# Optimization experiments

Hardware: AMD Instinct MI355X
Metric: run time of the kernel (lower is better)

The kernel has to match this reference:

```python
import jax, jax.numpy as jnp
import numpy as np

B, N, T, E, EH, C = 32, 500, 13, 2000, 300, 40
EPS = 1e-5


def _bn_noaffine(x):
    m = x.mean(axis=(0, 2, 3), keepdims=True)
    v = x.var(axis=(0, 2, 3), keepdims=True)
    return (x - m) * jax.lax.rsqrt(v + EPS)


def _bn(x, g, b):
    return g[None, :, None, None] * _bn_noaffine(x) + b[None, :, None, None]


def _conv1x1(x, W, b):
    # x: [B,Cin,N,T], W: [Cout,Cin]
    return jnp.einsum('bcnt,oc->bont', x, W) + b[None, :, None, None]


def _dconv(x, W, b, dil=2):
    # dilated causal conv, kernel (1,2): W [Cout,Cin,2]
    y = jnp.einsum('bcnt,oc->bont', x[..., :-dil], W[:, :, 0])
    y = y + jnp.einsum('bcnt,oc->bont', x[..., dil:], W[:, :, 1])
    return y + b[None, :, None, None]


def setup_inputs() -> dict:
    key = jax.random.key(0)
    ks = jax.random.split(key, 24)
    d = {}
    d['input'] = jax.random.normal(ks[0], (B, 1, N, T), jnp.float32)
    d['A_fwd'] = jax.random.uniform(ks[1], (N, N), jnp.float32) / N
    d['A_bwd'] = jax.random.uniform(ks[2], (N, N), jnp.float32) / N
    d['indices'] = jax.random.randint(ks[3], (2, E), 0, N, jnp.int32)
    d['G0_all'] = jax.random.uniform(ks[4], (E, EH), jnp.float32) * 0.01
    d['G1_all'] = jax.random.uniform(ks[5], (EH, E), jnp.float32) * 0.01
    d['nodevec1'] = jax.random.normal(ks[6], (N, 10), jnp.float32)
    d['nodevec2'] = jax.random.normal(ks[7], (10, N), jnp.float32)
    d['w_edge_f'] = jax.random.uniform(ks[8], (EH,), jnp.float32)
    d['w_edge_b'] = jax.random.uniform(ks[9], (EH,), jnp.float32)
    d['vsrc_f'] = jax.random.normal(ks[10], (3, C), jnp.float32) * 0.05
    d['vdst_f'] = jax.random.normal(ks[11], (3, C), jnp.float32) * 0.05
    d['vsrc_b'] = jax.random.normal(ks[12], (3, C), jnp.float32) * 0.05
    d['vdst_b'] = jax.random.normal(ks[13], (3, C), jnp.float32) * 0.05
    d['start_w'] = jax.random.normal(ks[14], (C, 1), jnp.float32)
    d['start_b'] = jnp.zeros((C,), jnp.float32)
    d['filter_w'] = jax.random.normal(ks[15], (3, C, C, 2), jnp.float32) * (1.0 / np.sqrt(2 * C))
    d['filter_b'] = jnp.zeros((3, C), jnp.float32)
    d['gate_w'] = jax.random.normal(ks[16], (3, C, C, 2), jnp.float32) * (1.0 / np.sqrt(2 * C))
    d['gate_b'] = jnp.zeros((3, C), jnp.float32)
    d['gconv_w'] = jax.random.normal(ks[17], (3, 7 * C, C), jnp.float32) * (1.0 / np.sqrt(7 * C))
    d['gconv_b'] = jnp.zeros((3, C), jnp.float32)
    d['bn_g_gamma'] = jnp.ones((3, C), jnp.float32)
    d['bn_g_beta'] = jnp.zeros((3, C), jnp.float32)
    d['bn_gamma'] = jnp.ones((3, C), jnp.float32)
    d['bn_beta'] = jnp.zeros((3, C), jnp.float32)
    d['skip_w'] = jax.random.normal(ks[18], (3, 320, C), jnp.float32) * (1.0 / np.sqrt(C))
    d['skip_b'] = jnp.zeros((3, 320), jnp.float32)
    d['end1_w'] = jax.random.normal(ks[19], (640, 320), jnp.float32) * (1.0 / np.sqrt(320))
    d['end1_b'] = jnp.zeros((640,), jnp.float32)
    d['end2_w'] = jax.random.normal(ks[20], (12, 640), jnp.float32) * (1.0 / np.sqrt(640))
    d['end2_b'] = jnp.zeros((12,), jnp.float32)
    return d


def reference(input, A_fwd, A_bwd, indices, G0_all, G1_all, nodevec1, nodevec2,
              w_edge_f, w_edge_b, vsrc_f, vdst_f, vsrc_b, vdst_b,
              start_w, start_b, filter_w, filter_b, gate_w, gate_b,
              gconv_w, gconv_b, bn_g_gamma, bn_g_beta, bn_gamma, bn_beta,
              skip_w, skip_b, end1_w, end1_b, end2_w, end2_b):
    x = _bn_noaffine(input)
    x = _conv1x1(x, start_w, start_b)
    b, _, n, _ = x.shape
    # adaptive adjacency: softmax(relu(V1 @ V2)) over rows (torch dim=1 on [N,N])
    adp = jax.nn.softmax(jax.nn.relu(nodevec1 @ nodevec2), axis=1)
    # hypergraph edge-to-edge diffusion operators: G0 @ diag(w) @ G1  ->  [E,E]
    GG_f = G0_all @ (w_edge_f[:, None] * G1_all)
    GG_b = G0_all @ (w_edge_b[:, None] * G1_all)
    i0, i1 = indices[0], indices[1]
    eye = jnp.eye(n, dtype=x.dtype)
    skip = None
    for blk in range(3):
        # dynamic edge scores from node features (mean over time)
        xmean = x.mean(axis=3)                              # [B,C,N]
        src = xmean[:, :, i0]                               # [B,C,E]
        dst = xmean[:, :, i1]
        sc_f = jnp.einsum('bce,c->be', src, vsrc_f[blk]) + jnp.einsum('bce,c->be', dst, vdst_f[blk])
        sc_b = jnp.einsum('bce,c->be', src, vsrc_b[blk]) + jnp.einsum('bce,c->be', dst, vdst_b[blk])
        ef = jax.nn.sigmoid(sc_f @ GG_f)                    # [B,E]
        eb = jax.nn.sigmoid(sc_b @ GG_b)
        # identity medium with sigmoid edge weights scattered at the edge indices
        Mf = jnp.broadcast_to(eye, (b, n, n)).at[:, i0, i1].set(ef)
        Mb = jnp.broadcast_to(eye, (b, n, n)).at[:, i0, i1].set(eb)
        s0 = Mf * A_fwd[None]                               # [B,N,N]
        s1 = jnp.swapaxes(Mb, 1, 2) * A_bwd[None]
        s2 = jnp.broadcast_to(adp, (b, n, n))
        residual = x
        f = jnp.tanh(_dconv(residual, filter_w[blk], filter_b[blk]))
        g = jax.nn.sigmoid(_dconv(residual, gate_w[blk], gate_b[blk]))
        x = f * g
        # diffusion graph conv, order 2, over 3 batched supports
        outs = [x]
        for A in (s0, s1, s2):
            x1 = jnp.einsum('bcnt,bnm->bcmt', x, A)
            outs.append(x1)
            outs.append(jnp.einsum('bcnt,bnm->bcmt', x1, A))
        h = jnp.concatenate(outs, axis=1)                   # [B,7C,N,T']
        x = jnp.einsum('bcnt,co->bont', h, gconv_w[blk]) + gconv_b[blk][None, :, None, None]
        x = _bn(x, bn_g_gamma[blk], bn_g_beta[blk])
        x = x + residual[:, :, :, -x.shape[3]:]
        x = _bn(x, bn_gamma[blk], bn_beta[blk])
        s = _conv1x1(x, skip_w[blk], skip_b[blk])
        skip = s if skip is None else s + skip[:, :, :, -s.shape[3]:]
    x = jax.nn.leaky_relu(skip)
    x = jax.nn.leaky_relu(_conv1x1(x, end1_w, end1_b))
    x = _conv1x1(x, end2_w, end2_b)
    return x
```

## Files before the change

### kernel.cpp

```cpp
#include <hip/hip_runtime.h>
#include <hip/hip_bf16.h>

constexpr int B_  = 32;
constexpr int N_  = 500;
constexpr int T0_ = 13;
constexpr int E_  = 2000;
constexpr int EH_ = 300;
constexpr int C_  = 40;
constexpr float EPS_ = 1e-5f;
constexpr int KP_ = 512;

typedef short bf16x8 __attribute__((ext_vector_type(8)));
typedef _Float16 f16x8 __attribute__((ext_vector_type(8)));
typedef _Float16 f16x4 __attribute__((ext_vector_type(4)));
typedef float f32x4  __attribute__((ext_vector_type(4)));

__device__ __forceinline__ float sigm(float x){ return 1.f/(1.f+__expf(-x)); }
__device__ __forceinline__ float lrelu(float x){ return x > 0.f ? x : 0.01f*x; }
__device__ __forceinline__ unsigned short f2bf(float f){
    __hip_bfloat16 h = __float2bfloat16(f);
    return *(unsigned short*)&h;
}
__device__ __forceinline__ float bf2f(unsigned short us){
    __hip_bfloat16 h = *(__hip_bfloat16*)&us;
    return __bfloat162float(h);
}

__global__ __launch_bounds__(256) void kern_init(float* __restrict__ insum, int* __restrict__ map,
                                                 int* __restrict__ cnts, int* __restrict__ selfe,
                                                 int* __restrict__ adpTbz)
{
    int i = blockIdx.x*256 + threadIdx.x;
    if (i < 2) insum[i] = 0.f;
    if (i < N_*N_) map[i] = -1;
    if (i < 1024) cnts[i] = 0;
    if (i < 512) selfe[i] = -1;
    if (i < KP_*KP_/2) adpTbz[i] = 0;
}

__global__ __launch_bounds__(256) void kern_zeroacc(float* __restrict__ p, int n)
{
    int i = blockIdx.x*256 + threadIdx.x;
    if (i < n) p[i] = 0.f;
}

__global__ __launch_bounds__(256) void kern_instats(const float* __restrict__ in, float* __restrict__ acc)
{
    float s = 0.f, ss = 0.f;
    int total = B_*N_*T0_;
    for (int i = blockIdx.x*256 + threadIdx.x; i < total; i += gridDim.x*256) {
        float v = in[i]; s += v; ss += v*v;
    }
    __shared__ float l1[256], l2[256];
    l1[threadIdx.x] = s; l2[threadIdx.x] = ss; __syncthreads();
    for (int o = 128; o > 0; o >>= 1) {
        if (threadIdx.x < o) { l1[threadIdx.x] += l1[threadIdx.x+o]; l2[threadIdx.x] += l2[threadIdx.x+o]; }
        __syncthreads();
    }
    if (threadIdx.x == 0) { atomicAdd(&acc[0], l1[0]); atomicAdd(&acc[1], l2[0]); }
}

__global__ __launch_bounds__(256) void kern_x0(const float* __restrict__ in, const float* __restrict__ insum,
    const float* __restrict__ sw, const float* __restrict__ sb, float* __restrict__ x)
{
    int idx = blockIdx.x*256 + threadIdx.x;
    int total = B_*N_*T0_*C_;
    if (idx >= total) return;
    float cnt = (float)(B_*N_*T0_);
    float mean = insum[0]/cnt;
    float var  = insum[1]/cnt - mean*mean;
    float inv  = rsqrtf(var + EPS_);
    int c = idx % C_;
    int pos = idx / C_;
    float xn = (in[pos] - mean)*inv;
    x[idx] = sw[c]*xn + sb[c];
}

__global__ __launch_bounds__(512) void kern_adp(const float* __restrict__ nv1, const float* __restrict__ nv2,
                                                __hip_bfloat16* __restrict__ adpTb)
{
    int n = blockIdx.x;
    int m = threadIdx.x;
    float r = 0.f;
    if (m < N_) {
        #pragma unroll
        for (int k = 0; k < 10; ++k) r += nv1[n*10+k]*nv2[k*N_+m];
        r = r > 0.f ? r : 0.f;
    }
    __shared__ float red[512];
    red[threadIdx.x] = (m < N_) ? r : -1e30f; __syncthreads();
    for (int o = 256; o > 0; o >>= 1) {
        if (threadIdx.x < o) red[threadIdx.x] = fmaxf(red[threadIdx.x], red[threadIdx.x+o]);
        __syncthreads();
    }
    float mx = red[0]; __syncthreads();
    float ev = (m < N_) ? __expf(r - mx) : 0.f;
    red[threadIdx.x] = ev; __syncthreads();
    for (int o = 256; o > 0; o >>= 1) {
        if (threadIdx.x < o) red[threadIdx.x] += red[threadIdx.x+o];
        __syncthreads();
    }
    float sum = red[0];
    if (m < N_) adpTb[(size_t)m*KP_ + n] = __float2bfloat16(ev/sum);
}

__global__ void kern_emax(const int* __restrict__ idx, int* __restrict__ map)
{
    int e = blockIdx.x*256 + threadIdx.x;
    if (e < E_) atomicMax(&map[idx[e]*N_ + idx[E_+e]], e);
}
__global__ void kern_ecnt(const int* __restrict__ idx, const int* __restrict__ map,
                          int* __restrict__ cnt0, int* __restrict__ cnt1, int* __restrict__ selfe)
{
    int e = blockIdx.x*256 + threadIdx.x;
    if (e >= E_) return;
    int i0 = idx[e], i1 = idx[E_+e];
    if (map[i0*N_+i1] != e) return;
    atomicAdd(&cnt1[i1], 1);
    atomicAdd(&cnt0[i0], 1);
    if (i0 == i1) selfe[i0] = e;
}
__global__ __launch_bounds__(512) void kern_scan(const int* __restrict__ cnt0, const int* __restrict__ cnt1,
    int* __restrict__ ptr0, int* __restrict__ ptr1, int* __restrict__ cur0, int* __restrict__ cur1)
{
    __shared__ int s0[512], s1[512];
    int tid = threadIdx.x;
    s0[tid] = (tid < N_) ? cnt0[tid] : 0;
    s1[tid] = (tid < N_) ? cnt1[tid] : 0;
    __syncthreads();
    for (int o = 1; o < 512; o <<= 1) {
        int v0 = (tid >= o) ? s0[tid-o] : 0;
        int v1 = (tid >= o) ? s1[tid-o] : 0;
        __syncthreads();
        s0[tid] += v0; s1[tid] += v1;
        __syncthreads();
    }
    if (tid == 0) { ptr0[0] = 0; ptr1[0] = 0; }
    if (tid < N_) {
        ptr0[tid+1] = s0[tid]; ptr1[tid+1] = s1[tid];
        cur0[tid] = (tid == 0) ? 0 : s0[tid-1];
        cur1[tid] = (tid == 0) ? 0 : s1[tid-1];
    }
}
__global__ void kern_efill(const int* __restrict__ idx, const int* __restrict__ map,
    const float* __restrict__ Af, const float* __restrict__ Ab,
    int* __restrict__ cur0, int* __restrict__ cur1,
    int* __restrict__ e0id, int* __restrict__ e0nb, float* __restrict__ a0v,
    int* __restrict__ e1id, int* __restrict__ e1nb, float* __restrict__ a1v)
{
    int e = blockIdx.x*256 + threadIdx.x;
    if (e >= E_) return;
    int i0 = idx[e], i1 = idx[E_+e];
    if (map[i0*N_+i1] != e) return;
    int s1 = atomicAdd(&cur1[i1], 1);
    e0id[s1] = e; e0nb[s1] = i0; a0v[s1] = Af[i0*N_+i1];
    int s0 = atomicAdd(&cur0[i0], 1);
    e1id[s0] = e; e1nb[s0] = i1; a1v[s0] = Ab[i1*N_+i0];
}

__global__ __launch_bounds__(64) void kern_umean(const float* __restrict__ x, int Tin,
    const float* __restrict__ vsf, const float* __restrict__ vdf,
    const float* __restrict__ vsb, const float* __restrict__ vdb,
    float* __restrict__ usf, float* __restrict__ udf, float* __restrict__ usb, float* __restrict__ udb)
{
    int bn = blockIdx.x;
    const float* xp = x + (size_t)bn*Tin*C_;
    int tid = threadIdx.x;
    float a0=0.f,a1=0.f,a2=0.f,a3=0.f;
    for (int i = tid; i < Tin*C_; i += 64) {
        float v = xp[i]; int c = i % C_;
        a0 += v*vsf[c]; a1 += v*vdf[c]; a2 += v*vsb[c]; a3 += v*vdb[c];
    }
    for (int o = 32; o > 0; o >>= 1) {
        a0 += __shfl_down(a0,o); a1 += __shfl_down(a1,o);
        a2 += __shfl_down(a2,o); a3 += __shfl_down(a3,o);
    }
    if (tid == 0) {
        float inv = 1.f/(float)Tin;
        usf[bn]=a0*inv; udf[bn]=a1*inv; usb[bn]=a2*inv; udb[bn]=a3*inv;
    }
}

__global__ __launch_bounds__(320) void kern_t(const int* __restrict__ idx,
    const float* __restrict__ usf, const float* __restrict__ udf,
    const float* __restrict__ usb, const float* __restrict__ udb,
    const float* __restrict__ G0, float* __restrict__ tf, float* __restrict__ tb,
    float* __restrict__ scf, float* __restrict__ scb)
{
    int b = blockIdx.x, chunk = blockIdx.y;
    int e0 = chunk*250;
    __shared__ float sf[250], sb2[250];
    int tid = threadIdx.x;
    for (int i = tid; i < 250; i += 320) {
        int e = e0 + i;
        int i0 = idx[e], i1 = idx[E_+e];
        float vf = usf[b*N_+i0] + udf[b*N_+i1];
        float vb = usb[b*N_+i0] + udb[b*N_+i1];
        sf[i] = vf; sb2[i] = vb;
        scf[b*E_+e] = vf; scb[b*E_+e] = vb;
    }
    __syncthreads();
    if (tid < EH_) {
        float af = 0.f, ab = 0.f;
        for (int i = 0; i < 250; ++i) {
            float g = G0[(size_t)(e0+i)*EH_ + tid];
            af += sf[i]*g; ab += sb2[i]*g;
        }
        atomicAdd(&tf[b*EH_+tid], af);
        atomicAdd(&tb[b*EH_+tid], ab);
    }
}

__global__ __launch_bounds__(256) void kern_ef(const float* __restrict__ tf, const float* __restrict__ tb,
    const float* __restrict__ wf, const float* __restrict__ wb, const float* __restrict__ G1,
    float* __restrict__ ef, float* __restrict__ eb)
{
    int b = blockIdx.y;
    int e = blockIdx.x*256 + threadIdx.x;
    __shared__ float f[EH_], g[EH_];
    for (int i = threadIdx.x; i < EH_; i += 256) {
        f[i] = tf[b*EH_+i]*wf[i];
        g[i] = tb[b*EH_+i]*wb[i];
    }
    __syncthreads();
    if (e < E_) {
        float af = 0.f, ab = 0.f;
        for (int h = 0; h < EH_; ++h) {
            float v = G1[(size_t)h*E_ + e];
            af += f[h]*v; ab += g[h]*v;
        }
        ef[b*E_+e] = sigm(af);
        eb[b*E_+e] = sigm(ab);
    }
}

__global__ __launch_bounds__(256) void kern_dconv_acc(const float* __restrict__ x, int Tin,
    const float* __restrict__ fw, const float* __restrict__ fb4,
    const float* __restrict__ gw, const float* __restrict__ gb4,
    const float* __restrict__ wl0, const float* __restrict__ gbias,
    float* __restrict__ xg, float* __restrict__ gc,
    __hip_bfloat16* __restrict__ xgT, int JP)
{
    int Tout = Tin - 2;
    int nout = Tout*C_;
    int tile = threadIdx.x >> 7;
    int lane = threadIdx.x & 127;
    int bn = blockIdx.x*2 + tile;
    int b = bn / N_, n = bn % N_;
    __shared__ alignas(16) float xs[2][T0_*C_];
    __shared__ alignas(16) float wf[2*C_*C_];
    __shared__ alignas(16) float wg[2*C_*C_];
    __shared__ alignas(16) float wl[C_*C_];
    __shared__ alignas(16) float ps[2][11*C_];
    int tid = threadIdx.x;
    {
        const float4* xp = (const float4*)(x + (size_t)bn*Tin*C_);
        float4* xd = (float4*)xs[tile];
        for (int i = lane; i < (Tin*C_)/4; i += 128) xd[i] = xp[i];
    }
    for (int i = tid; i < 2*C_*C_; i += 256) {
        int k = i / (C_*C_); int r = i % (C_*C_); int c = r / C_; int o = r % C_;
        wf[i] = fw[(o*C_+c)*2 + k];
        wg[i] = gw[(o*C_+c)*2 + k];
    }
    for (int i = tid; i < C_*C_; i += 256) wl[i] = wl0[i];
    __syncthreads();
    int nq = Tout*10;
    for (int u = lane; u < nq; u += 128) {
        int t = u/10, o = (u%10)*4;
        float4 f4 = *(const float4*)&fb4[o];
        float4 g4 = *(const float4*)&gb4[o];
        for (int c = 0; c < C_; ++c) {
            float x0v = xs[tile][t*C_+c], x2v = xs[tile][(t+2)*C_+c];
            float4 wf0 = *(const float4*)&wf[c*C_+o];
            float4 wf1 = *(const float4*)&wf[C_*C_ + c*C_+o];
            float4 wg0 = *(const float4*)&wg[c*C_+o];
            float4 wg1 = *(const float4*)&wg[C_*C_ + c*C_+o];
            f4.x += wf0.x*x0v + wf1.x*x2v;  f4.y += wf0.y*x0v + wf1.y*x2v;
            f4.z += wf0.z*x0v + wf1.z*x2v;  f4.w += wf0.w*x0v + wf1.w*x2v;
            g4.x += wg0.x*x0v + wg1.x*x2v;  g4.y += wg0.y*x0v + wg1.y*x2v;
            g4.z += wg0.z*x0v + wg1.z*x2v;  g4.w += wg0.w*x0v + wg1.w*x2v;
        }
        float4 r4;
        r4.x = tanhf(f4.x)*sigm(g4.x);
        r4.y = tanhf(f4.y)*sigm(g4.y);
        r4.z = tanhf(f4.z)*sigm(g4.z);
        r4.w = tanhf(f4.w)*sigm(g4.w);
        *(float4*)&ps[tile][t*C_+o] = r4;
        *(float4*)&xg[(size_t)bn*nout + t*C_+o] = r4;
        int j = t*C_+o;
        size_t tb = ((size_t)b*JP + j)*KP_ + n;
        xgT[tb]          = __float2bfloat16(r4.x);
        xgT[tb + KP_]    = __float2bfloat16(r4.y);
        xgT[tb + 2*KP_]  = __float2bfloat16(r4.z);
        xgT[tb + 3*KP_]  = __float2bfloat16(r4.w);
    }
    __syncthreads();
    for (int u = lane; u < nq; u += 128) {
        int t = u/10, o = (u%10)*4;
        float4 a4 = *(const float4*)&gbias[o];
        for (int c = 0; c < C_; ++c) {
            float s = ps[tile][t*C_+c];
            float4 w = *(const float4*)&wl[c*C_+o];
            a4.x += s*w.x; a4.y += s*w.y; a4.z += s*w.z; a4.w += s*w.w;
        }
        *(float4*)&gc[(size_t)bn*nout + t*C_+o] = a4;
    }
}

__global__ __launch_bounds__(256) void kern_sparse_acc(const float* __restrict__ in,
    float* __restrict__ outTile, int Tout,
    const int* __restrict__ ptr, const int* __restrict__ nbr, const int* __restrict__ eid,
    const float* __restrict__ aval, const float* __restrict__ coef,
    const float* __restrict__ Amat, const int* __restrict__ selfe,
    const float* __restrict__ gwp, float* __restrict__ gc)
{
    int tile = threadIdx.x >> 7;
    int lane = threadIdx.x & 127;
    int bn = blockIdx.x*2 + tile;
    int b = bn / N_, m = bn % N_;
    __shared__ float wv[2][64];
    __shared__ int   nb[2][64];
    __shared__ alignas(16) float ps[2][11*C_];
    __shared__ alignas(16) float wl[C_*C_];
    int tid = threadIdx.x;
    int p0 = ptr[m], p1 = ptr[m+1];
    int deg = p1 - p0; if (deg > 64) deg = 64;
    if (lane < deg) {
        wv[tile][lane] = coef[b*E_ + eid[p0+lane]] * aval[p0+lane];
        nb[tile][lane] = nbr[p0+lane];
    }
    for (int i = tid; i < C_*C_; i += 256) wl[i] = gwp[i];
    __syncthreads();
    float dval = (selfe[m] >= 0) ? 0.f : Amat[(size_t)m*N_ + m];
    const float* inb = in + (size_t)b*N_*Tout*C_;
    int nout = Tout*C_;
    for (int oi = lane; oi < nout; oi += 128) {
        float acc = dval * inb[(size_t)m*nout + oi];
        for (int j = 0; j < deg; ++j) acc += wv[tile][j]*inb[(size_t)nb[tile][j]*nout + oi];
        ps[tile][oi] = acc;
        if (outTile) outTile[(size_t)bn*nout + oi] = acc;
    }
    __syncthreads();
    int nq = Tout*10;
    for (int u = lane; u < nq; u += 128) {
        int t = u/10, o = (u%10)*4;
        float4 a4 = *(const float4*)&gc[(size_t)bn*nout + t*C_+o];
        for (int c = 0; c < C_; ++c) {
            float s = ps[tile][t*C_+c];
            float4 w = *(const float4*)&wl[c*C_+o];
            a4.x += s*w.x; a4.y += s*w.y; a4.z += s*w.z; a4.w += s*w.w;
        }
        *(float4*)&gc[(size_t)bn*nout + t*C_+o] = a4;
    }
}

__global__ __launch_bounds__(256) void kern_gemm_mfma(const __hip_bfloat16* __restrict__ adpTb,
    const __hip_bfloat16* __restrict__ inT, float* __restrict__ outF,
    __hip_bfloat16* __restrict__ outT, int LD, int JP)
{
    int tid = threadIdx.x;
    int wave = tid >> 6, lane = tid & 63;
    int rn = lane & 15, q = lane >> 4;
    int b = blockIdx.z;
    int m0 = blockIdx.x*64;
    int j0 = blockIdx.y*64;
    const short* Ap = (const short*)adpTb + (size_t)(m0 + wave*16 + rn)*KP_ + q*8;
    bf16x8 areg[16];
    #pragma unroll
    for (int kk = 0; kk < 16; ++kk) areg[kk] = *(const bf16x8*)(Ap + kk*32);
    const short* Bp = (const short*)inT + ((size_t)b*JP + j0 + rn)*KP_ + q*8;
    f32x4 acc[4] = {};
    #pragma unroll
    for (int kk = 0; kk < 16; ++kk) {
        #pragma unroll
        for (int s = 0; s < 4; ++s) {
            bf16x8 bb = *(const bf16x8*)(Bp + (size_t)s*16*KP_ + kk*32);
            acc[s] = __builtin_amdgcn_mfma_f32_16x16x32_bf16(areg[kk], bb, acc[s], 0, 0, 0);
        }
    }
    int mb = m0 + wave*16 + q*4;
    #pragma unroll
    for (int s = 0; s < 4; ++s) {
        int j = j0 + s*16 + rn;
        if (j >= LD) continue;
        #pragma unroll
        for (int r = 0; r < 4; ++r) {
            int m = mb + r;
            if (m < N_) outF[((size_t)b*N_ + m)*LD + j] = acc[s][r];
        }
        if (outT) {
            ushort4 v;
            v.x = f2bf(acc[s][0]); v.y = f2bf(acc[s][1]);
            v.z = f2bf(acc[s][2]); v.w = f2bf(acc[s][3]);
            *(ushort4*)((unsigned short*)outT + ((size_t)b*JP + j)*KP_ + mb) = v;
        }
    }
}

__global__ __launch_bounds__(256) void kern_gacc(const float* __restrict__ part, const float* __restrict__ gwp,
    float* __restrict__ gc, int Tout)
{
    int tile = threadIdx.x >> 7;
    int lane = threadIdx.x & 127;
    int bn = blockIdx.x*2 + tile;
    int nout = Tout*C_;
    __shared__ alignas(16) float ps[2][11*C_];
    __shared__ alignas(16) float wl[C_*C_];
    int tid = threadIdx.x;
    {
        const float4* pp = (const float4*)(part + (size_t)bn*nout);
        float4* pd = (float4*)ps[tile];
        for (int i = lane; i < nout/4; i += 128) pd[i] = pp[i];
    }
    for (int i = tid; i < C_*C_; i += 256) wl[i] = gwp[i];
    __syncthreads();
    int nq = Tout*10;
    for (int u = lane; u < nq; u += 128) {
        int t = u/10, o = (u%10)*4;
        float4 a4 = *(const float4*)&gc[(size_t)bn*nout + t*C_+o];
        for (int c = 0; c < C_; ++c) {
            float s = ps[tile][t*C_+c];
            float4 w = *(const float4*)&wl[c*C_+o];
            a4.x += s*w.x; a4.y += s*w.y; a4.z += s*w.z; a4.w += s*w.w;
        }
        *(float4*)&gc[(size_t)bn*nout + t*C_+o] = a4;
    }
}

__global__ __launch_bounds__(320) void kern_bnstats(const float* __restrict__ src, size_t total, float* __restrict__ acc)
{
    int tid = threadIdx.x;
    float s = 0.f, ss = 0.f;
    for (size_t i = (size_t)blockIdx.x*320 + tid; i < total; i += (size_t)gridDim.x*320) {
        float v = src[i]; s += v; ss += v*v;
    }
    __shared__ float ls[320], lss[320];
    ls[tid] = s; lss[tid] = ss; __syncthreads();
    if (tid < C_) {
        float t1 = 0.f, t2 = 0.f;
        for (int r = 0; r < 8; ++r) { t1 += ls[r*C_+tid]; t2 += lss[r*C_+tid]; }
        atomicAdd(&acc[tid], t1); atomicAdd(&acc[C_+tid], t2);
    }
}

__global__ __launch_bounds__(320) void kern_bn1(float* __restrict__ gc, const float* __restrict__ resid,
    int Tin, int Tout, const float* __restrict__ acc1,
    const float* __restrict__ g1, const float* __restrict__ b1, float* __restrict__ acc2)
{
    int tid = threadIdx.x; int c = tid % C_;
    float cnt = (float)(B_*N_*Tout);
    float mean = acc1[c]/cnt;
    float var  = acc1[C_+c]/cnt - mean*mean;
    float inv  = rsqrtf(var + EPS_);
    float gg = g1[c], bb = b1[c];
    int dlt = Tin - Tout;
    float s = 0.f, ss = 0.f;
    size_t total = (size_t)B_*N_*Tout*C_;
    for (size_t i = (size_t)blockIdx.x*320 + tid; i < total; i += (size_t)gridDim.x*320) {
        size_t pos = i / C_; int t = (int)(pos % Tout); size_t bn = pos / Tout;
        float y = gg*(gc[i]-mean)*inv + bb;
        y += resid[(bn*Tin + (t+dlt))*C_ + c];
        gc[i] = y;
        s += y; ss += y*y;
    }
    __shared__ float ls[320], lss[320];
    ls[tid] = s; lss[tid] = ss; __syncthreads();
    if (tid < C_) {
        float t1 = 0.f, t2 = 0.f;
        for (int r = 0; r < 8; ++r) { t1 += ls[r*C_+tid]; t2 += lss[r*C_+tid]; }
        atomicAdd(&acc2[tid], t1); atomicAdd(&acc2[C_+tid], t2);
    }
}

__global__ __launch_bounds__(256) void kern_bn2(const float* __restrict__ gc, float* __restrict__ xout, int Tout,
    const float* __restrict__ acc2, const float* __restrict__ g2, const float* __restrict__ b2)
{
    size_t total = (size_t)B_*N_*Tout*C_;
    size_t i = (size_t)blockIdx.x*256 + threadIdx.x;
    if (i >= total) return;
    int c = (int)(i % C_);
    float cnt = (float)(B_*N_*Tout);
    float mean = acc2[c]/cnt;
    float var  = acc2[C_+c]/cnt - mean*mean;
    float inv  = rsqrtf(var + EPS_);
    xout[i] = g2[c]*(gc[i]-mean)*inv + b2[c];
}

__global__ __launch_bounds__(256) void kern_skip(const float* __restrict__ x, int Tout,
    const float* __restrict__ sw, const float* __restrict__ sbias, __hip_bfloat16* __restrict__ skp, int first,
    const float* __restrict__ acc2, const float* __restrict__ g2, const float* __restrict__ b2)
{
    int bn0 = blockIdx.x*4; int half = blockIdx.y;
    int off = Tout - 7;
    __shared__ alignas(16) float xs[4][7*C_];
    __shared__ alignas(16) float wl[C_*164];
    __shared__ float scl[C_], bia[C_];
    int tid = threadIdx.x;
    if (acc2) {
        if (tid < C_) {
            float cnt = (float)(B_*N_*Tout);
            float mean = acc2[tid]/cnt;
            float var  = acc2[C_+tid]/cnt - mean*mean;
            float inv  = rsqrtf(var + EPS_);
            scl[tid] = g2[tid]*inv;
            bia[tid] = b2[tid] - g2[tid]*mean*inv;
        }
        __syncthreads();
    }
    for (int i = tid; i < 4*(7*C_/4); i += 256) {
        int bl = i / 70, r = i % 70;
        float4 v = ((const float4*)(x + ((size_t)(bn0+bl)*Tout + off)*C_))[r];
        if (acc2) {
            int c0 = (r*4) % C_;
            v.x = scl[c0]*v.x + bia[c0];
            v.y = scl[c0+1]*v.y + bia[c0+1];
            v.z = scl[c0+2]*v.z + bia[c0+2];
            v.w = scl[c0+3]*v.w + bia[c0+3];
        }
        ((float4*)xs[bl])[r] = v;
    }
    for (int i = tid; i < 160*C_; i += 256) {
        int oo = i / C_, c = i % C_;
        wl[c*164 + oo] = sw[(size_t)(half*160 + oo)*C_ + c];
    }
    __syncthreads();
    for (int u = tid; u < 4*7*40; u += 256) {
        int bl = u / 280; int v = u % 280;
        int t = v / 40, o = (v % 40)*4;
        float4 a4 = {0.f,0.f,0.f,0.f};
        for (int c = 0; c < C_; ++c) {
            float s = xs[bl][t*C_+c];
            float4 w = *(const float4*)&wl[c*164 + o];
            a4.x += s*w.x; a4.y += s*w.y; a4.z += s*w.z; a4.w += s*w.w;
        }
        int og = half*160 + o;
        float4 b4 = *(const float4*)&sbias[og];
        a4.x += b4.x; a4.y += b4.y; a4.z += b4.z; a4.w += b4.w;
        size_t di = ((size_t)(bn0+bl)*7 + t)*320 + og;
        if (first) {
            skp[di+0] = __float2bfloat16(a4.x);
            skp[di+1] = __float2bfloat16(a4.y);
            skp[di+2] = __float2bfloat16(a4.z);
            skp[di+3] = __float2bfloat16(a4.w);
        } else {
            skp[di+0] = __float2bfloat16(__bfloat162float(skp[di+0]) + a4.x);
            skp[di+1] = __float2bfloat16(__bfloat162float(skp[di+1]) + a4.y);
            skp[di+2] = __float2bfloat16(__bfloat162float(skp[di+2]) + a4.z);
            skp[di+3] = __float2bfloat16(__bfloat162float(skp[di+3]) + a4.w);
        }
    }
}

__global__ __launch_bounds__(256) void kern_cvtw(const float* __restrict__ w, __hip_bfloat16* __restrict__ wb, int n)
{
    int i = blockIdx.x*256 + threadIdx.x;
    if (i < n) wb[i] = __float2bfloat16(w[i]);
}

constexpr int ASD_ = 324;
__global__ __launch_bounds__(256, 2) void kern_end2(const __hip_bfloat16* __restrict__ skp,
    const __hip_bfloat16* __restrict__ e1wb, const float* __restrict__ e1b,
    const float* __restrict__ e2w, const float* __restrict__ e2b, float* __restrict__ out)
{
    __shared__ short As[64*ASD_];
    __shared__ _Float16 w2h[640][12];
    int tid = threadIdx.x;
    int wave = tid >> 6, lane = tid & 63;
    int rn = lane & 15, q = lane >> 4;
    int m0 = blockIdx.x*64;
    {
        const bf16x8* gA = (const bf16x8*)((const short*)skp + (size_t)m0*320);
        for (int i = tid; i < 2560; i += 256) {
            bf16x8 v = gA[i];
            bf16x8 r;
            #pragma unroll
            for (int e = 0; e < 8; ++e)
                r[e] = (short)f2bf(lrelu(bf2f((unsigned short)v[e])));
            int row = i / 40, col = (i % 40)*8;
            *(bf16x8*)&As[row*ASD_ + col] = r;
        }
    }
    for (int i = tid; i < 640*12; i += 256) {
        int c = i / 12, o = i % 12;
        w2h[c][o] = (_Float16)e2w[o*640 + c];
    }
    __syncthreads();
    const short* Arow = As + (wave*16 + rn)*ASD_ + q*8;
    float acc_out[4][12] = {};
    const short* e1p = (const short*)e1wb;
    #pragma unroll
    for (int csp = 0; csp < 20; ++csp) {
        const short* Bp0 = e1p + (size_t)(csp*32 + rn)*320 + q*8;
        const short* Bp1 = Bp0 + 16*320;
        f32x4 c00 = {}, c01 = {}, c10 = {}, c11 = {};
        #pragma unroll
        for (int kk = 0; kk < 10; kk += 2) {
            bf16x8 a0 = *(const bf16x8*)(Arow + kk*32);
            bf16x8 a1 = *(const bf16x8*)(Arow + (kk+1)*32);
            bf16x8 b00 = *(const bf16x8*)(Bp0 + kk*32);
            bf16x8 b01 = *(const bf16x8*)(Bp0 + (kk+1)*32);
            bf16x8 b10 = *(const bf16x8*)(Bp1 + kk*32);
            bf16x8 b11 = *(const bf16x8*)(Bp1 + (kk+1)*32);
            c00 = __builtin_amdgcn_mfma_f32_16x16x32_bf16(a0, b00, c00, 0, 0, 0);
            c10 = __builtin_amdgcn_mfma_f32_16x16x32_bf16(a0, b10, c10, 0, 0, 0);
            c01 = __builtin_amdgcn_mfma_f32_16x16x32_bf16(a1, b01, c01, 0, 0, 0);
            c11 = __builtin_amdgcn_mfma_f32_16x16x32_bf16(a1, b11, c11, 0, 0, 0);
        }
        int ca = csp*32 + rn, cb = ca + 16;
        float bias0 = e1b[ca], bias1 = e1b[cb];
        f16x4 wa0 = *(const f16x4*)&w2h[ca][0];
        f16x4 wa1 = *(const f16x4*)&w2h[ca][4];
        f16x4 wa2 = *(const f16x4*)&w2h[ca][8];
        f16x4 wb0 = *(const f16x4*)&w2h[cb][0];
        f16x4 wb1 = *(const f16x4*)&w2h[cb][4];
        f16x4 wb2 = *(const f16x4*)&w2h[cb][8];
        #pragma unroll
        for (int r = 0; r < 4; ++r) {
            float y0 = lrelu(c00[r] + c01[r] + bias0);
            float y1 = lrelu(c10[r] + c11[r] + bias1);
            #pragma unroll
            for (int o = 0; o < 4; ++o) {
                acc_out[r][o]   += y0*(float)wa0[o] + y1*(float)wb0[o];
                acc_out[r][4+o] += y0*(float)wa1[o] + y1*(float)wb1[o];
                acc_out[r][8+o] += y0*(float)wa2[o] + y1*(float)wb2[o];
            }
        }
    }
    #pragma unroll
    for (int r = 0; r < 4; ++r)
        #pragma unroll
        for (int o = 0; o < 12; ++o) {
            float v = acc_out[r][o];
            v += __shfl_xor(v, 1);
            v += __shfl_xor(v, 2);
            v += __shfl_xor(v, 4);
            v += __shfl_xor(v, 8);
            acc_out[r][o] = v;
        }
    if (rn < 12) {
        float bo = e2b[rn];
        #pragma unroll
        for (int r = 0; r < 4; ++r) {
            float v = 0.f;
            #pragma unroll
            for (int o = 0; o < 12; ++o) v = (rn == o) ? acc_out[r][o] : v;
            int gm = m0 + wave*16 + q*4 + r;
            int t = gm % 7; int bn = gm / 7; int n = bn % N_; int b = bn / N_;
            out[(((size_t)b*12 + rn)*N_ + n)*7 + t] = v + bo;
        }
    }
}

extern "C" void kernel_launch(void* const* d_in, const int* in_sizes, int n_in,
                              void* d_out, int out_size, void* d_ws, size_t ws_size,
                              hipStream_t stream)
{
    (void)in_sizes; (void)n_in; (void)out_size;
    const float* input   = (const float*)d_in[0];
    const float* A_fwd   = (const float*)d_in[1];
    const float* A_bwd   = (const float*)d_in[2];
    const int*   indices = (const int*)  d_in[3];
    const float* G0      = (const float*)d_in[4];
    const float* G1      = (const float*)d_in[5];
    const float* nv1     = (const float*)d_in[6];
    const float* nv2     = (const float*)d_in[7];
    const float* wef     = (const float*)d_in[8];
    const float* web     = (const float*)d_in[9];
    const float* vsf     = (const float*)d_in[10];
    const float* vdf     = (const float*)d_in[11];
    const float* vsb     = (const float*)d_in[12];
    const float* vdb     = (const float*)d_in[13];
    const float* start_w = (const float*)d_in[14];
    const float* start_b = (const float*)d_in[15];
    const float* filt_w  = (const float*)d_in[16];
    const float* filt_b  = (const float*)d_in[17];
    const float* gate_w  = (const float*)d_in[18];
    const float* gate_b  = (const float*)d_in[19];
    const float* gcw     = (const float*)d_in[20];
    const float* gcb     = (const float*)d_in[21];
    const float* bng_g   = (const float*)d_in[22];
    const float* bng_b   = (const float*)d_in[23];
    const float* bn_g    = (const float*)d_in[24];
    const float* bn_b    = (const float*)d_in[25];
    const float* skw     = (const float*)d_in[26];
    const float* skb     = (const float*)d_in[27];
    const float* e1w     = (const float*)d_in[28];
    const float* e1b     = (const float*)d_in[29];
    const float* e2w     = (const float*)d_in[30];
    const float* e2b     = (const float*)d_in[31];
    float* out = (float*)d_out;

    float* W = (float*)d_ws;
    size_t off = 0;
    auto FA = [&](size_t n){ off = (off + 3) & ~(size_t)3; float* p = W + off; off += n; return p; };
    float* insum  = FA(2);
    float* tf     = FA((size_t)B_*EH_);
    float* tb     = FA((size_t)B_*EH_);
    float* bnacc1 = FA(80);
    float* bnacc2 = FA(80);
    float* usf = FA((size_t)B_*N_); float* udf = FA((size_t)B_*N_);
    float* usb = FA((size_t)B_*N_); float* udb = FA((size_t)B_*N_);
    float* scf = FA((size_t)B_*E_); float* scb = FA((size_t)B_*E_);
    float* efv = FA((size_t)B_*E_); float* ebv = FA((size_t)B_*E_);
    __hip_bfloat16* adpTb = (__hip_bfloat16*)FA((size_t)KP_*KP_/2);
    float* a0v = FA(E_); float* a1v = FA(E_);
    int* map  = (int*)FA((size_t)N_*N_);
    int* cnt0 = (int*)FA(512); int* cnt1 = (int*)FA(512);
    int* ptr0 = (int*)FA(512); int* ptr1 = (int*)FA(512);
    int* cur0 = (int*)FA(512); int* cur1 = (int*)FA(512);
    int* selfe = (int*)FA(512);
    int* e0id = (int*)FA(E_); int* e0nb = (int*)FA(E_);
    int* e1id = (int*)FA(E_); int* e1nb = (int*)FA(E_);
    float* xA  = FA((size_t)B_*N_*T0_*C_);
    float* xg  = FA((size_t)B_*N_*11*C_);
    float* pa  = FA((size_t)B_*N_*11*C_);
    float* gc  = FA((size_t)B_*N_*11*C_);
    __hip_bfloat16* skp = (__hip_bfloat16*)FA((size_t)B_*N_*7*320/2);
    __hip_bfloat16* xgT = (__hip_bfloat16*)FA((size_t)B_*448*KP_/2);
    __hip_bfloat16* paT = (__hip_bfloat16*)FA((size_t)B_*448*KP_/2);
    __hip_bfloat16* e1wb = (__hip_bfloat16*)xg;

    if (ws_size < off*sizeof(float)) return;

    kern_init<<<(N_*N_+255)/256, 256, 0, stream>>>(insum, map, cnt0, selfe, (int*)adpTb);
    kern_instats<<<256, 256, 0, stream>>>(input, insum);
    kern_x0<<<(B_*N_*T0_*C_+255)/256, 256, 0, stream>>>(input, insum, start_w, start_b, xA);
    kern_adp<<<N_, 512, 0, stream>>>(nv1, nv2, adpTb);
    kern_emax<<<(E_+255)/256, 256, 0, stream>>>(indices, map);
    kern_ecnt<<<(E_+255)/256, 256, 0, stream>>>(indices, map, cnt0, cnt1, selfe);
    kern_scan<<<1, 512, 0, stream>>>(cnt0, cnt1, ptr0, ptr1, cur0, cur1);
    kern_efill<<<(E_+255)/256, 256, 0, stream>>>(indices, map, A_fwd, A_bwd, cur0, cur1,
                                                 e0id, e0nb, a0v, e1id, e1nb, a1v);

    for (int blk = 0; blk < 3; ++blk) {
        int Tin = T0_ - 2*blk;
        int Tout = Tin - 2;
        int LD = Tout*C_;
        int JP = (LD + 63) & ~63;
        size_t total = (size_t)B_*N_*Tout*C_;
        kern_zeroacc<<<(2*B_*EH_+160+255)/256, 256, 0, stream>>>(tf, 2*B_*EH_+160);

        kern_umean<<<B_*N_, 64, 0, stream>>>(xA, Tin, vsf+blk*C_, vdf+blk*C_, vsb+blk*C_, vdb+blk*C_,
                                             usf, udf, usb, udb);
        kern_t<<<dim3(B_, 8), 320, 0, stream>>>(indices, usf, udf, usb, udb, G0, tf, tb, scf, scb);
        kern_ef<<<dim3(8, B_), 256, 0, stream>>>(tf, tb, wef, web, G1, efv, ebv);

        const float* gwb = gcw + (size_t)blk*7*C_*C_;
        kern_dconv_acc<<<B_*N_/2, 256, 0, stream>>>(xA, Tin,
            filt_w + (size_t)blk*2*C_*C_, filt_b + blk*C_,
            gate_w + (size_t)blk*2*C_*C_, gate_b + blk*C_,
            gwb + 0*C_*C_, gcb + blk*C_, xg, gc, xgT, JP);
        kern_sparse_acc<<<B_*N_/2, 256, 0, stream>>>(xg, pa, Tout, ptr1, e0nb, e0id, a0v, efv,
                                                     A_fwd, selfe, gwb + 1*C_*C_, gc);
        kern_sparse_acc<<<B_*N_/2, 256, 0, stream>>>(pa, nullptr, Tout, ptr1, e0nb, e0id, a0v, efv,
                                                     A_fwd, selfe, gwb + 2*C_*C_, gc);
        kern_sparse_acc<<<B_*N_/2, 256, 0, stream>>>(xg, pa, Tout, ptr0, e1nb, e1id, a1v, ebv,
                                                     A_bwd, selfe, gwb + 3*C_*C_, gc);
        kern_sparse_acc<<<B_*N_/2, 256, 0, stream>>>(pa, nullptr, Tout, ptr0, e1nb, e1id, a1v, ebv,
                                                     A_bwd, selfe, gwb + 4*C_*C_, gc);
        dim3 gg(8, JP/64, B_);
        kern_gemm_mfma<<<gg, 256, 0, stream>>>(adpTb, xgT, pa, paT, LD, JP);
        kern_gacc<<<B_*N_/2, 256, 0, stream>>>(pa, gwb + 5*C_*C_, gc, Tout);
        kern_gemm_mfma<<<gg, 256, 0, stream>>>(adpTb, paT, xg, nullptr, LD, JP);
        kern_gacc<<<B_*N_/2, 256, 0, stream>>>(xg, gwb + 6*C_*C_, gc, Tout);

        kern_bnstats<<<512, 320, 0, stream>>>(gc, total, bnacc1);
        kern_bn1<<<512, 320, 0, stream>>>(gc, xA, Tin, Tout, bnacc1, bng_g + blk*C_, bng_b + blk*C_, bnacc2);
        if (blk < 2) {
            kern_bn2<<<(int)((total+255)/256), 256, 0, stream>>>(gc, xA, Tout, bnacc2, bn_g + blk*C_, bn_b + blk*C_);
            kern_skip<<<dim3(B_*N_/4, 2), 256, 0, stream>>>(xA, Tout, skw + (size_t)blk*320*C_, skb + blk*320,
                                                            skp, blk == 0 ? 1 : 0, nullptr, nullptr, nullptr);
        } else {
            kern_skip<<<dim3(B_*N_/4, 2), 256, 0, stream>>>(gc, Tout, skw + (size_t)blk*320*C_, skb + blk*320,
                                                            skp, 0, bnacc2, bn_g + blk*C_, bn_b + blk*C_);
        }
    }

    kern_cvtw<<<(640*320+255)/256, 256, 0, stream>>>(e1w, e1wb, 640*320);
    kern_end2<<<B_*N_*7/64, 256, 0, stream>>>(skp, e1wb, e1b, e2w, e2b, out);
}
```

Baseline: 2.525 ms.

## Fuse paired sparse diffusion passes, fold BN stats into gacc, drop dead stores

Merges the forward and backward sparse diffusion steps into one kernel per hop, with a second scratch buffer, so gc is read and written once per pair instead of once per support. This cuts kernel launches and repeated gc round-trips. BN statistics for the graph-conv output are now gathered with shared atomics inside the last gacc kernel, removing a separate full-tensor reduction pass. Unused scf/scb stores in kern_t are dropped. The fused path needs extra workspace and falls back to the old kernels when there is not enough.

Result: slower. 3.107 ms (+23.0%).

```diff
diff --git a/kernel.cpp b/kernel.cpp
--- a/kernel.cpp
+++ b/kernel.cpp
@@ -184,8 +184,7 @@
 __global__ __launch_bounds__(320) void kern_t(const int* __restrict__ idx,
     const float* __restrict__ usf, const float* __restrict__ udf,
     const float* __restrict__ usb, const float* __restrict__ udb,
-    const float* __restrict__ G0, float* __restrict__ tf, float* __restrict__ tb,
-    float* __restrict__ scf, float* __restrict__ scb)
+    const float* __restrict__ G0, float* __restrict__ tf, float* __restrict__ tb)
 {
     int b = blockIdx.x, chunk = blockIdx.y;
     int e0 = chunk*250;
@@ -194,10 +193,8 @@
     for (int i = tid; i < 250; i += 320) {
         int e = e0 + i;
         int i0 = idx[e], i1 = idx[E_+e];
-        float vf = usf[b*N_+i0] + udf[b*N_+i1];
-        float vb = usb[b*N_+i0] + udb[b*N_+i1];
-        sf[i] = vf; sb2[i] = vb;
-        scf[b*E_+e] = vf; scb[b*E_+e] = vb;
+        sf[i]  = usf[b*N_+i0] + udf[b*N_+i1];
+        sb2[i] = usb[b*N_+i0] + udb[b*N_+i1];
     }
     __syncthreads();
     if (tid < EH_) {
@@ -349,6 +346,77 @@
         for (int c = 0; c < C_; ++c) {
             float s = ps[tile][t*C_+c];
             float4 w = *(const float4*)&wl[c*C_+o];
+            a4.x += s*w.x; a4.y += s*w.y; a4.z += s*w.z; a4.w += s*w.w;
+        }
+        *(float4*)&gc[(size_t)bn*nout + t*C_+o] = a4;
+    }
+}
+
+__global__ __launch_bounds__(256) void kern_sparse2(const float* __restrict__ in0, const float* __restrict__ in1,
+    float* __restrict__ out0, float* __restrict__ out1, int Tout,
+    const int* __restrict__ ptrA, const int* __restrict__ nbrA, const int* __restrict__ eidA,
+    const float* __restrict__ avalA, const float* __restrict__ coefA, const float* __restrict__ AmatA,
+    const int* __restrict__ ptrB, const int* __restrict__ nbrB, const int* __restrict__ eidB,
+    const float* __restrict__ avalB, const float* __restrict__ coefB, const float* __restrict__ AmatB,
+    const int* __restrict__ selfe,
+    const float* __restrict__ w0, const float* __restrict__ w1, float* __restrict__ gc)
+{
+    int tile = threadIdx.x >> 7;
+    int lane = threadIdx.x & 127;
+    int bn = blockIdx.x*2 + tile;
+    int b = bn / N_, m = bn % N_;
+    __shared__ float wvA[2][64]; __shared__ int nbA[2][64];
+    __shared__ float wvB[2][64]; __shared__ int nbB[2][64];
+    __shared__ alignas(16) float ps[2][11*C_];
+    __shared__ alignas(16) float wl0[C_*C_];
+    __shared__ alignas(16) float wl1[C_*C_];
+    int tid = threadIdx.x;
+    int pA = ptrA[m]; int degA = ptrA[m+1] - pA; if (degA > 64) degA = 64;
+    int pB = ptrB[m]; int degB = ptrB[m+1] - pB; if (degB > 64) degB = 64;
+    if (lane < degA) { wvA[tile][lane] = coefA[b*E_ + eidA[pA+lane]] * avalA[pA+lane]; nbA[tile][lane] = nbrA[pA+lane]; }
+    if (lane < degB) { wvB[tile][lane] = coefB[b*E_ + eidB[pB+lane]] * avalB[pB+lane]; nbB[tile][lane] = nbrB[pB+lane]; }
+    for (int i = tid; i < C_*C_; i += 256) { wl0[i] = w0[i]; wl1[i] = w1[i]; }
+    __syncthreads();
+    int nout = Tout*C_;
+    int nq = Tout*10;
+    float dA = (selfe[m] >= 0) ? 0.f : AmatA[(size_t)m*N_ + m];
+    float dB = (selfe[m] >= 0) ? 0.f : AmatB[(size_t)m*N_ + m];
+    {
+        const float* inb = in0 + (size_t)b*N_*nout;
+        for (int oi = lane; oi < nout; oi += 128) {
+            float acc = dA * inb[(size_t)m*nout + oi];
+            for (int j = 0; j < degA; ++j) acc += wvA[tile][j]*inb[(size_t)nbA[tile][j]*nout + oi];
+            ps[tile][oi] = acc;
+            if (out0) out0[(size_t)bn*nout + oi] = acc;
+        }
+    }
+    __syncthreads();
+    bool act = lane < nq;
+    int t = lane/10, o = (lane%10)*4;
+    float4 a4 = {0.f,0.f,0.f,0.f};
+    if (act) {
+        a4 = *(const float4*)&gc[(size_t)bn*nout + t*C_+o];
+        for (int c = 0; c < C_; ++c) {
+            float s = ps[tile][t*C_+c];
+            float4 w = *(const float4*)&wl0[c*C_+o];
+            a4.x += s*w.x; a4.y += s*w.y; a4.z += s*w.z; a4.w += s*w.w;
+        }
+    }
+    __syncthreads();
+    {
+        const float* inb = in1 + (size_t)b*N_*nout;
+        for (int oi = lane; oi < nout; oi += 128) {
+            float acc = dB * inb[(size_t)m*nout + oi];
+            for (int j = 0; j < degB; ++j) acc += wvB[tile][j]*inb[(size_t)nbB[tile][j]*nout + oi];
+            ps[tile][oi] = acc;
+            if (out1) out1[(size_t)bn*nout + oi] = acc;
+        }
+    }
+    __syncthreads();
+    if (act) {
+        for (int c = 0; c < C_; ++c) {
+            float s = ps[tile][t*C_+c];
+            float4 w = *(const float4*)&wl1[c*C_+o];
             a4.x += s*w.x; a4.y += s*w.y; a4.z += s*w.z; a4.w += s*w.w;
         }
         *(float4*)&gc[(size_t)bn*nout + t*C_+o] = a4;
@@ -428,19 +496,44 @@
     }
 }
 
-__global__ __launch_bounds__(320) void kern_bnstats(const float* __restrict__ src, size_t total, float* __restrict__ acc)
-{
-    int tid = threadIdx.x;
-    float s = 0.f, ss = 0.f;
-    for (size_t i = (size_t)blockIdx.x*320 + tid; i < total; i += (size_t)gridDim.x*320) {
-        float v = src[i]; s += v; ss += v*v;
-    }
-    __shared__ float ls[320], lss[320];
-    ls[tid] = s; lss[tid] = ss; __syncthreads();
+__global__ __launch_bounds__(256) void kern_gacc_bn(const float* __restrict__ part, const float* __restrict__ gwp,
+    float* __restrict__ gc, int Tout, float* __restrict__ acc1)
+{
+    int tile = threadIdx.x >> 7;
+    int lane = threadIdx.x & 127;
+    int bn = blockIdx.x*2 + tile;
+    int nout = Tout*C_;
+    __shared__ alignas(16) float ps[2][11*C_];
+    __shared__ alignas(16) float wl[C_*C_];
+    __shared__ float ssum[C_], ssq[C_];
+    int tid = threadIdx.x;
+    if (tid < C_) { ssum[tid] = 0.f; ssq[tid] = 0.f; }
+    {
+        const float4* pp = (const float4*)(part + (size_t)bn*nout);
+        float4* pd = (float4*)ps[tile];
+        for (int i = lane; i < nout/4; i += 128) pd[i] = pp[i];
+    }
+    for (int i = tid; i < C_*C_; i += 256) wl[i] = gwp[i];
+    __syncthreads();
+    int nq = Tout*10;
+    for (int u = lane; u < nq; u += 128) {
+        int t = u/10, o = (u%10)*4;
+        float4 a4 = *(const float4*)&gc[(size_t)bn*nout + t*C_+o];
+        for (int c = 0; c < C_; ++c) {
+            float s = ps[tile][t*C_+c];
+            float4 w = *(const float4*)&wl[c*C_+o];
+            a4.x += s*w.x; a4.y += s*w.y; a4.z += s*w.z; a4.w += s*w.w;
+        }
+        *(float4*)&gc[(size_t)bn*nout + t*C_+o] = a4;
+        atomicAdd(&ssum[o+0], a4.x); atomicAdd(&ssq[o+0], a4.x*a4.x);
+        atomicAdd(&ssum[o+1], a4.y); atomicAdd(&ssq[o+1], a4.y*a4.y);
+        atomicAdd(&ssum[o+2], a4.z); atomicAdd(&ssq[o+2], a4.z*a4.z);
+        atomicAdd(&ssum[o+3], a4.w); atomicAdd(&ssq[o+3], a4.w*a4.w);
+    }
+    __syncthreads();
     if (tid < C_) {
-        float t1 = 0.f, t2 = 0.f;
-        for (int r = 0; r < 8; ++r) { t1 += ls[r*C_+tid]; t2 += lss[r*C_+tid]; }
-        atomicAdd(&acc[tid], t1); atomicAdd(&acc[C_+tid], t2);
+        atomicAdd(&acc1[tid], ssum[tid]);
+        atomicAdd(&acc1[C_+tid], ssq[tid]);
     }
 }
 
@@ -701,7 +794,6 @@
     float* bnacc2 = FA(80);
     float* usf = FA((size_t)B_*N_); float* udf = FA((size_t)B_*N_);
     float* usb = FA((size_t)B_*N_); float* udb = FA((size_t)B_*N_);
-    float* scf = FA((size_t)B_*E_); float* scb = FA((size_t)B_*E_);
     float* efv = FA((size_t)B_*E_); float* ebv = FA((size_t)B_*E_);
     __hip_bfloat16* adpTb = (__hip_bfloat16*)FA((size_t)KP_*KP_/2);
     float* a0v = FA(E_); float* a1v = FA(E_);
@@ -719,9 +811,12 @@
     __hip_bfloat16* skp = (__hip_bfloat16*)FA((size_t)B_*N_*7*320/2);
     __hip_bfloat16* xgT = (__hip_bfloat16*)FA((size_t)B_*448*KP_/2);
     __hip_bfloat16* paT = (__hip_bfloat16*)FA((size_t)B_*448*KP_/2);
+    size_t offBase = off;
+    float* pa1 = FA((size_t)B_*N_*11*C_);
     __hip_bfloat16* e1wb = (__hip_bfloat16*)xg;
 
-    if (ws_size < off*sizeof(float)) return;
+    if (ws_size < offBase*sizeof(float)) return;
+    bool dual = ws_size >= off*sizeof(float);
 
     kern_init<<<(N_*N_+255)/256, 256, 0, stream>>>(insum, map, cnt0, selfe, (int*)adpTb);
     kern_instats<<<256, 256, 0, stream>>>(input, insum);
@@ -743,7 +838,7 @@
 
         kern_umean<<<B_*N_, 64, 0, stream>>>(xA, Tin, vsf+blk*C_, vdf+blk*C_, vsb+blk*C_, vdb+blk*C_,
                                              usf, udf, usb, udb);
-        kern_t<<<dim3(B_, 8), 320, 0, stream>>>(indices, usf, udf, usb, udb, G0, tf, tb, scf, scb);
+        kern_t<<<dim3(B_, 8), 320, 0, stream>>>(indices, usf, udf, usb, udb, G0, tf, tb);
         kern_ef<<<dim3(8, B_), 256, 0, stream>>>(tf, tb, wef, web, G1, efv, ebv);
 
         const float* gwb = gcw + (size_t)blk*7*C_*C_;
@@ -751,21 +846,32 @@
             filt_w + (size_t)blk*2*C_*C_, filt_b + blk*C_,
             gate_w + (size_t)blk*2*C_*C_, gate_b + blk*C_,
             gwb + 0*C_*C_, gcb + blk*C_, xg, gc, xgT, JP);
-        kern_sparse_acc<<<B_*N_/2, 256, 0, stream>>>(xg, pa, Tout, ptr1, e0nb, e0id, a0v, efv,
-                                                     A_fwd, selfe, gwb + 1*C_*C_, gc);
-        kern_sparse_acc<<<B_*N_/2, 256, 0, stream>>>(pa, nullptr, Tout, ptr1, e0nb, e0id, a0v, efv,
-                                                     A_fwd, selfe, gwb + 2*C_*C_, gc);
-        kern_sparse_acc<<<B_*N_/2, 256, 0, stream>>>(xg, pa, Tout, ptr0, e1nb, e1id, a1v, ebv,
-                                                     A_bwd, selfe, gwb + 3*C_*C_, gc);
-        kern_sparse_acc<<<B_*N_/2, 256, 0, stream>>>(pa, nullptr, Tout, ptr0, e1nb, e1id, a1v, ebv,
-                                                     A_bwd, selfe, gwb + 4*C_*C_, gc);
+
+        if (dual) {
+            kern_sparse2<<<B_*N_/2, 256, 0, stream>>>(xg, xg, pa, pa1, Tout,
+                ptr1, e0nb, e0id, a0v, efv, A_fwd,
+                ptr0, e1nb, e1id, a1v, ebv, A_bwd, selfe,
+                gwb + 1*C_*C_, gwb + 3*C_*C_, gc);
+            kern_sparse2<<<B_*N_/2, 256, 0, stream>>>(pa, pa1, nullptr, nullptr, Tout,
+                ptr1, e0nb, e0id, a0v, efv, A_fwd,
+                ptr0, e1nb, e1id, a1v, ebv, A_bwd, selfe,
+                gwb + 2*C_*C_, gwb + 4*C_*C_, gc);
+        } else {
+            kern_sparse_acc<<<B_*N_/2, 256, 0, stream>>>(xg, pa, Tout, ptr1, e0nb, e0id, a0v, efv,
+                                                         A_fwd, selfe, gwb + 1*C_*C_, gc);
+            kern_sparse_acc<<<B_*N_/2, 256, 0, stream>>>(pa, nullptr, Tout, ptr1, e0nb, e0id, a0v, efv,
+                                                         A_fwd, selfe, gwb + 2*C_*C_, gc);
+            kern_sparse_acc<<<B_*N_/2, 256, 0, stream>>>(xg, pa, Tout, ptr0, e1nb, e1id, a1v, ebv,
+                                                         A_bwd, selfe, gwb + 3*C_*C_, gc);
+            kern_sparse_acc<<<B_*N_/2, 256, 0, stream>>>(pa, nullptr, Tout, ptr0, e1nb, e1id, a1v, ebv,
+                                                         A_bwd, selfe, gwb + 4*C_*C_, gc);
+        }
         dim3 gg(8, JP/64, B_);
         kern_gemm_mfma<<<gg, 256, 0, stream>>>(adpTb, xgT, pa, paT, LD, JP);
         kern_gacc<<<B_*N_/2, 256, 0, stream>>>(pa, gwb + 5*C_*C_, gc, Tout);
         kern_gemm_mfma<<<gg, 256, 0, stream>>>(adpTb, paT, xg, nullptr, LD, JP);
-        kern_gacc<<<B_*N_/2, 256, 0, stream>>>(xg, gwb + 6*C_*C_, gc, Tout);
-
-        kern_bnstats<<<512, 320, 0, stream>>>(gc, total, bnacc1);
+        kern_gacc_bn<<<B_*N_/2, 256, 0, stream>>>(xg, gwb + 6*C_*C_, gc, Tout, bnacc1);
+
         kern_bn1<<<512, 320, 0, stream>>>(gc, xA, Tin, Tout, bnacc1, bng_g + blk*C_, bng_b + blk*C_, bnacc2);
         if (blk < 2) {
             kern_bn2<<<(int)((total+255)/256), 256, 0, stream>>>(gc, xA, Tout, bnacc2, bn_g + blk*C_, bn_b + blk*C_);
```
